# Optimization experiments

Measured on AMD Instinct MI355X. Metric: run time of the kernel, lower is better.

The kernel has to match this reference:

```python
import jax, jax.numpy as jnp
import numpy as np

EPS = 1e-6
L, H, D, DFF = 4, 6, 6, 64  # n_layers, num_heads(=dim, head_dim=1), d_hid, ffn hidden


def layernorm(x, w, b):
    mu = jnp.mean(x, axis=-1, keepdims=True)
    var = jnp.mean((x - mu) ** 2, axis=-1, keepdims=True)
    return (x - mu) / jnp.sqrt(var + EPS) * w + b


def autocorr(x, qw, qb, kw, kb, vw, vb, l1w, l1b):
    # x: [B,S,H]; head_dim==1 so per-head Linear is scalar w*x+b per head.
    k_in = jnp.concatenate([x[:, :1], x[:, :-1]], axis=1)   # roll right, first row kept
    v_in = jnp.concatenate([x[:, 1:], x[:, -1:]], axis=1)   # roll left, last row kept
    q = x * qw + qb
    k = k_in * kw + kb
    v = v_in * vw + vb
    teo = q * q - k * v                                      # [B,S,H]
    # nn.LayerNorm([1]) over size-1 axis: mean==x, var==0 -> output is bias
    normed = (teo - teo) / jnp.sqrt(EPS) * l1w + l1b
    scores = jax.nn.softmax(normed, axis=1)                  # over seq dim
    return scores * teo


def mha(x, p, li, ai):
    out = autocorr(x, p['qw'][li, ai], p['qb'][li, ai], p['kw'][li, ai],
                   p['kb'][li, ai], p['vw'][li, ai], p['vb'][li, ai],
                   p['ln1_w'][li, ai], p['ln1_b'][li, ai])
    return layernorm(out + x, p['mha_ln_w'][li, ai], p['mha_ln_b'][li, ai])


def setup_inputs() -> dict:
    key = jax.random.key(0)
    ks = jax.random.split(key, 24)
    n = jax.random.normal
    inp = {
        'x_batch': n(ks[0], (128, 4096, 6), jnp.float32),
        'enc_output': n(ks[1], (128, 4096, 6), jnp.float32),
        'dec_ln_w': jnp.ones((D,), jnp.float32),
        'dec_ln_b': jnp.zeros((D,), jnp.float32),
        'qw': n(ks[2], (L, 2, H), jnp.float32),
        'qb': n(ks[3], (L, 2, H), jnp.float32) * 0.1,
        'kw': n(ks[4], (L, 2, H), jnp.float32),
        'kb': n(ks[5], (L, 2, H), jnp.float32) * 0.1,
        'vw': n(ks[6], (L, 2, H), jnp.float32),
        'vb': n(ks[7], (L, 2, H), jnp.float32) * 0.1,
        'ln1_w': jnp.ones((L, 2), jnp.float32),
        'ln1_b': jnp.zeros((L, 2), jnp.float32),
        'mha_ln_w': jnp.ones((L, 2, D), jnp.float32),
        'mha_ln_b': jnp.zeros((L, 2, D), jnp.float32),
        'ffn_w1': n(ks[8], (L, DFF, D), jnp.float32) * (1.0 / np.sqrt(D)),
        'ffn_b1': jnp.zeros((L, DFF), jnp.float32),
        'ffn_w2': n(ks[9], (L, D, DFF), jnp.float32) * (1.0 / np.sqrt(DFF)),
        'ffn_b2': jnp.zeros((L, D), jnp.float32),
        'ffn_ln_w': jnp.ones((L, D), jnp.float32),
        'ffn_ln_b': jnp.zeros((L, D), jnp.float32),
    }
    return inp


def reference(x_batch, enc_output, dec_ln_w, dec_ln_b, qw, qb, kw, kb, vw, vb,
              ln1_w, ln1_b, mha_ln_w, mha_ln_b, ffn_w1, ffn_b1, ffn_w2, ffn_b2,
              ffn_ln_w, ffn_ln_b):
    p = dict(qw=qw, qb=qb, kw=kw, kb=kb, vw=vw, vb=vb, ln1_w=ln1_w, ln1_b=ln1_b,
             mha_ln_w=mha_ln_w, mha_ln_b=mha_ln_b)
    x = layernorm(x_batch, dec_ln_w, dec_ln_b)  # dropout p=0 -> identity
    for li in range(L):
        x = mha(x, p, li, 0)   # self-attention block
        x = mha(x, p, li, 1)   # "enc" attention block (also self, per source)
        h = jax.nn.relu(jnp.einsum('bsd,fd->bsf', x, ffn_w1[li]) + ffn_b1[li])
        y = jnp.einsum('bsf,df->bsd', h, ffn_w2[li]) + ffn_b2[li] + x
        x = layernorm(y, ffn_ln_w[li], ffn_ln_b[li])
    return x
```

## Files before the change

### kernel.cpp

```cpp
#include <hip/hip_runtime.h>

#define S_LEN  4096
#define DM     6
#define NLAYER 4
#define NFF    64
#define HALO   8
#define TPB    128
#define OUT_PER_WAVE 112
#define BLK_X 19

typedef float    vf2 __attribute__((ext_vector_type(2)));
typedef float    vf4 __attribute__((ext_vector_type(4)));
typedef _Float16 vh4 __attribute__((ext_vector_type(4)));
typedef _Float16 vh8 __attribute__((ext_vector_type(8)));

#define XSZ (128*16)
#define YSTRIDE 132
#define YSZ (DM*YSTRIDE*4)
#define WAVE_LDS (XSZ + YSZ)

__device__ __forceinline__ vf2 splat2(float s){ vf2 r; r.x = s; r.y = s; return r; }
__device__ __forceinline__ unsigned pkh(float a, float b){
    return __builtin_bit_cast(unsigned, __builtin_amdgcn_cvt_pkrtz(a, b));
}

__device__ __forceinline__ void ln6v(vf2* v, const float* __restrict__ w,
                                     const float* __restrict__ b) {
    vf2 mu = (((v[0]+v[1])+(v[2]+v[3]))+(v[4]+v[5])) * (1.0f/6.0f);
    vf2 var = splat2(0.0f);
#pragma unroll
    for (int d = 0; d < DM; ++d) { vf2 dd = v[d]-mu; var = __builtin_elementwise_fma(dd, dd, var); }
    vf2 a = var * (1.0f/6.0f) + splat2(1e-6f);
    vf2 r; r.x = rsqrtf(a.x); r.y = rsqrtf(a.y);
#pragma unroll
    for (int d = 0; d < DM; ++d)
        v[d] = __builtin_elementwise_fma((v[d]-mu)*r, splat2(w[d]), splat2(b[d]));
}

__global__ __launch_bounds__(TPB, 5)
void decoder_fused(const float* __restrict__ x_batch,
                   const float* __restrict__ dec_ln_w, const float* __restrict__ dec_ln_b,
                   const float* __restrict__ qw, const float* __restrict__ qb,
                   const float* __restrict__ kw, const float* __restrict__ kb,
                   const float* __restrict__ vw, const float* __restrict__ vb,
                   const float* __restrict__ mha_ln_w, const float* __restrict__ mha_ln_b,
                   const float* __restrict__ ffn_w1, const float* __restrict__ ffn_b1,
                   const float* __restrict__ ffn_w2, const float* __restrict__ ffn_b2,
                   const float* __restrict__ ffn_ln_w, const float* __restrict__ ffn_ln_b,
                   float* __restrict__ out) {
    const int lane = threadIdx.x & 63;
    const int wid  = threadIdx.x >> 6;
    const int w    = blockIdx.x * (TPB/64) + wid;
    const int b    = blockIdx.y;
    const int p    = w * OUT_PER_WAVE - HALO + 2*lane;
    const int c    = lane & 15, g = lane >> 4;

    __shared__ __align__(16) char smem[(TPB/64) * WAVE_LDS];
    char* wbase = smem + wid * WAVE_LDS;
    char* Xb = wbase;
    char* Yb = wbase + XSZ;

    vf2 x2[DM];
    if (p >= 0 && p + 1 < S_LEN) {
        const float4* s = reinterpret_cast<const float4*>(x_batch + ((size_t)b*S_LEN + p)*DM);
        float4 a0 = s[0], a1 = s[1], a2 = s[2];
        x2[0].x=a0.x; x2[1].x=a0.y; x2[2].x=a0.z; x2[3].x=a0.w; x2[4].x=a1.x; x2[5].x=a1.y;
        x2[0].y=a1.z; x2[1].y=a1.w; x2[2].y=a2.x; x2[3].y=a2.y; x2[4].y=a2.z; x2[5].y=a2.w;
    } else {
        const int pc = min(max(p, 0), S_LEN-1);
        const float2* s = reinterpret_cast<const float2*>(x_batch + ((size_t)b*S_LEN + pc)*DM);
        float2 a0 = s[0], a1 = s[1], a2 = s[2];
        x2[0] = splat2(a0.x); x2[1] = splat2(a0.y); x2[2] = splat2(a1.x);
        x2[3] = splat2(a1.y); x2[4] = splat2(a2.x); x2[5] = splat2(a2.y);
    }

    ln6v(x2, dec_ln_w, dec_ln_b);

#pragma unroll 1
    for (int li = 0; li < NLAYER; ++li) {
        vh8 w1f[4]; vf4 b1f[4]; vh8 w2f[2];
#pragma unroll
        for (int mt = 0; mt < 4; ++mt) {
            uint4 ua = make_uint4(0u, 0u, 0u, 0u);
            if (g == 0) {
                const float* wr = ffn_w1 + li*NFF*DM + (mt*16 + c)*DM;
                float2 u0 = *reinterpret_cast<const float2*>(wr);
                float2 u1 = *reinterpret_cast<const float2*>(wr + 2);
                float2 u2 = *reinterpret_cast<const float2*>(wr + 4);
                ua = make_uint4(pkh(u0.x,u0.y), pkh(u1.x,u1.y), pkh(u2.x,u2.y), 0u);
            }
            w1f[mt] = __builtin_bit_cast(vh8, ua);

            float4 bb = *reinterpret_cast<const float4*>(ffn_b1 + li*NFF + mt*16 + g*4);
            vf4 bv; bv.x=bb.x; bv.y=bb.y; bv.z=bb.z; bv.w=bb.w;
            b1f[mt] = bv;
        }
#pragma unroll
        for (int ks = 0; ks < 2; ++ks) {
            uint4 uw = make_uint4(0u, 0u, 0u, 0u);
            if (c < DM) {
                const float* wr = ffn_w2 + li*DM*NFF + c*NFF + ks*32 + g*4;
                float4 a0 = *reinterpret_cast<const float4*>(wr);
                float4 a1 = *reinterpret_cast<const float4*>(wr + 16);
                uw = make_uint4(pkh(a0.x,a0.y), pkh(a0.z,a0.w), pkh(a1.x,a1.y), pkh(a1.z,a1.w));
            }
            w2f[ks] = __builtin_bit_cast(vh8, uw);
        }

#pragma unroll 1
        for (int ai = 0; ai < 2; ++ai) {
            const int base = (li*2 + ai) * DM;
            vf2 xm[DM], xp[DM];
#pragma unroll
            for (int d = 0; d < DM; ++d) {
                float up = __shfl_up (x2[d].y, 1);
                float dn = __shfl_down(x2[d].x, 1);
                xm[d].x = (p <= 0) ? x2[d].x : up;
                xm[d].y = x2[d].x;
                xp[d].x = x2[d].y;
                xp[d].y = (p + 1 >= S_LEN - 1) ? x2[d].y : dn;
            }
#pragma unroll
            for (int d = 0; d < DM; ++d) {
                vf2 q = __builtin_elementwise_fma(x2[d], splat2(qw[base+d]), splat2(qb[base+d]));
                vf2 k = __builtin_elementwise_fma(xm[d], splat2(kw[base+d]), splat2(kb[base+d]));
                vf2 v = __builtin_elementwise_fma(xp[d], splat2(vw[base+d]), splat2(vb[base+d]));
                vf2 teo = __builtin_elementwise_fma(q, q, -(k*v));
                x2[d] = __builtin_elementwise_fma(teo, splat2(1.0f/(float)S_LEN), x2[d]);
            }
            ln6v(x2, mha_ln_w + base, mha_ln_b + base);
        }

        {
            {
                char* r0 = Xb + lane*32;
                *(uint4*)r0      = make_uint4(pkh(x2[0].x,x2[1].x), pkh(x2[2].x,x2[3].x),
                                              pkh(x2[4].x,x2[5].x), 0u);
                *(uint4*)(r0+16) = make_uint4(pkh(x2[0].y,x2[1].y), pkh(x2[2].y,x2[3].y),
                                              pkh(x2[4].y,x2[5].y), 0u);
            }
#pragma unroll 2
            for (int t = 0; t < 8; ++t) {
                vh8 bfrag = (vh8)(_Float16)0;
                if (g == 0) bfrag = *(const vh8*)(Xb + (16*t + c)*16);

                vf4 yacc; yacc.x=0.f; yacc.y=0.f; yacc.z=0.f; yacc.w=0.f;
#pragma unroll
                for (int ks = 0; ks < 2; ++ks) {
                    vf4 h0 = __builtin_amdgcn_mfma_f32_16x16x32_f16(w1f[2*ks+0], bfrag, b1f[2*ks+0], 0, 0, 0);
                    vf4 h1 = __builtin_amdgcn_mfma_f32_16x16x32_f16(w1f[2*ks+1], bfrag, b1f[2*ks+1], 0, 0, 0);
                    uint4 hu = make_uint4(pkh(h0.x,h0.y), pkh(h0.z,h0.w),
                                          pkh(h1.x,h1.y), pkh(h1.z,h1.w));
                    vh8 hb = __builtin_bit_cast(vh8, hu);
                    hb = __builtin_elementwise_max(hb, (vh8)(_Float16)0);
                    yacc = __builtin_amdgcn_mfma_f32_16x16x32_f16(hb, w2f[ks], yacc, 0, 0, 0);
                }
                if (c < DM) {
                    float* yp = (float*)Yb + c*YSTRIDE + 16*t + g*4;
                    *reinterpret_cast<vf4*>(yp) = yacc;
                }
            }
            const float* b2 = ffn_b2 + li*DM;
#pragma unroll
            for (int d = 0; d < DM; ++d) {
                float2 yv = *(const float2*)((float*)Yb + d*YSTRIDE + 2*lane);
                vf2 t2; t2.x = yv.x; t2.y = yv.y;
                x2[d] = x2[d] + splat2(b2[d]) + t2;
            }
            ln6v(x2, ffn_ln_w + li*DM, ffn_ln_b + li*DM);
        }
    }

    if (lane >= 4 && lane < 60 && p < S_LEN) {
        float4* dst = reinterpret_cast<float4*>(out + ((size_t)b*S_LEN + p)*DM);
        float4 a0, a1, a2;
        a0.x=x2[0].x; a0.y=x2[1].x; a0.z=x2[2].x; a0.w=x2[3].x;
        a1.x=x2[4].x; a1.y=x2[5].x; a1.z=x2[0].y; a1.w=x2[1].y;
        a2.x=x2[2].y; a2.y=x2[3].y; a2.z=x2[4].y; a2.w=x2[5].y;
        dst[0]=a0; dst[1]=a1; dst[2]=a2;
    }
}

extern "C" void kernel_launch(void* const* d_in, const int* in_sizes, int n_in,
                              void* d_out, int out_size, void* d_ws, size_t ws_size,
                              hipStream_t stream) {
    const float* x_batch  = (const float*)d_in[0];
    const float* dec_ln_w = (const float*)d_in[2];
    const float* dec_ln_b = (const float*)d_in[3];
    const float* qw       = (const float*)d_in[4];
    const float* qb       = (const float*)d_in[5];
    const float* kw       = (const float*)d_in[6];
    const float* kb       = (const float*)d_in[7];
    const float* vw       = (const float*)d_in[8];
    const float* vb       = (const float*)d_in[9];
    const float* mha_ln_w = (const float*)d_in[12];
    const float* mha_ln_b = (const float*)d_in[13];
    const float* ffn_w1   = (const float*)d_in[14];
    const float* ffn_b1   = (const float*)d_in[15];
    const float* ffn_w2   = (const float*)d_in[16];
    const float* ffn_b2   = (const float*)d_in[17];
    const float* ffn_ln_w = (const float*)d_in[18];
    const float* ffn_ln_b = (const float*)d_in[19];
    float* out = (float*)d_out;

    const int B = in_sizes[0] / (S_LEN * DM);
    dim3 grid(BLK_X, B);
    decoder_fused<<<grid, TPB, 0, stream>>>(
        x_batch, dec_ln_w, dec_ln_b, qw, qb, kw, kb, vw, vb,
        mha_ln_w, mha_ln_b, ffn_w1, ffn_b1, ffn_w2, ffn_b2,
        ffn_ln_w, ffn_ln_b, out);
}
```

Baseline: 139.9 us.

## Switch to one token per lane and fold FFN bias into MFMA operand

Each lane now handles one sequence position instead of two, so a wave produces 48 outputs with an 8-token halo on each side instead of 112, and the grid grows to 43 blocks per row. The scalar path drops the packed float2 code, halves per-wave LDS and registers, and the launch bounds target 8 waves per SIMD instead of 5 to raise occupancy. The first FFN bias is folded into the MFMA by adding a constant-1 input column and a bias weight column, which removes the bias accumulator registers. In exchange, halo recomputation overhead rises from 16/128 to 16/64 of the work, and the bias is now rounded to fp16.

```diff
diff --git a/kernel.cpp b/kernel.cpp
--- a/kernel.cpp
+++ b/kernel.cpp
@@ -6,38 +6,35 @@
 #define NFF    64
 #define HALO   8
 #define TPB    128
-#define OUT_PER_WAVE 112
-#define BLK_X 19
+#define OUT_PER_WAVE 48
+#define WAVES_PER_ROW 86
+#define BLK_X 43
 
-typedef float    vf2 __attribute__((ext_vector_type(2)));
 typedef float    vf4 __attribute__((ext_vector_type(4)));
-typedef _Float16 vh4 __attribute__((ext_vector_type(4)));
 typedef _Float16 vh8 __attribute__((ext_vector_type(8)));
 
-#define XSZ (128*16)
-#define YSTRIDE 132
+#define XSZ (64*16)
+#define YSTRIDE 68
 #define YSZ (DM*YSTRIDE*4)
 #define WAVE_LDS (XSZ + YSZ)
 
-__device__ __forceinline__ vf2 splat2(float s){ vf2 r; r.x = s; r.y = s; return r; }
 __device__ __forceinline__ unsigned pkh(float a, float b){
     return __builtin_bit_cast(unsigned, __builtin_amdgcn_cvt_pkrtz(a, b));
 }
 
-__device__ __forceinline__ void ln6v(vf2* v, const float* __restrict__ w,
+__device__ __forceinline__ void ln6s(float* v, const float* __restrict__ w,
                                      const float* __restrict__ b) {
-    vf2 mu = (((v[0]+v[1])+(v[2]+v[3]))+(v[4]+v[5])) * (1.0f/6.0f);
-    vf2 var = splat2(0.0f);
+    float mu = (((v[0]+v[1])+(v[2]+v[3]))+(v[4]+v[5])) * (1.0f/6.0f);
+    float var = 0.0f;
 #pragma unroll
-    for (int d = 0; d < DM; ++d) { vf2 dd = v[d]-mu; var = __builtin_elementwise_fma(dd, dd, var); }
-    vf2 a = var * (1.0f/6.0f) + splat2(1e-6f);
-    vf2 r; r.x = rsqrtf(a.x); r.y = rsqrtf(a.y);
+    for (int d = 0; d < DM; ++d) { float dd = v[d]-mu; var = fmaf(dd, dd, var); }
+    float r = rsqrtf(var * (1.0f/6.0f) + 1e-6f);
 #pragma unroll
     for (int d = 0; d < DM; ++d)
-        v[d] = __builtin_elementwise_fma((v[d]-mu)*r, splat2(w[d]), splat2(b[d]));
+        v[d] = fmaf((v[d]-mu)*r, w[d], b[d]);
 }
 
-__global__ __launch_bounds__(TPB, 5)
+__global__ __launch_bounds__(TPB, 8)
 void decoder_fused(const float* __restrict__ x_batch,
                    const float* __restrict__ dec_ln_w, const float* __restrict__ dec_ln_b,
                    const float* __restrict__ qw, const float* __restrict__ qb,
@@ -52,7 +49,7 @@
     const int wid  = threadIdx.x >> 6;
     const int w    = blockIdx.x * (TPB/64) + wid;
     const int b    = blockIdx.y;
-    const int p    = w * OUT_PER_WAVE - HALO + 2*lane;
+    const int p    = w * OUT_PER_WAVE - HALO + lane;
     const int c    = lane & 15, g = lane >> 4;
 
     __shared__ __align__(16) char smem[(TPB/64) * WAVE_LDS];
@@ -60,25 +57,19 @@
     char* Xb = wbase;
     char* Yb = wbase + XSZ;
 
-    vf2 x2[DM];
-    if (p >= 0 && p + 1 < S_LEN) {
-        const float4* s = reinterpret_cast<const float4*>(x_batch + ((size_t)b*S_LEN + p)*DM);
-        float4 a0 = s[0], a1 = s[1], a2 = s[2];
-        x2[0].x=a0.x; x2[1].x=a0.y; x2[2].x=a0.z; x2[3].x=a0.w; x2[4].x=a1.x; x2[5].x=a1.y;
-        x2[0].y=a1.z; x2[1].y=a1.w; x2[2].y=a2.x; x2[3].y=a2.y; x2[4].y=a2.z; x2[5].y=a2.w;
-    } else {
+    float x[DM];
+    {
         const int pc = min(max(p, 0), S_LEN-1);
         const float2* s = reinterpret_cast<const float2*>(x_batch + ((size_t)b*S_LEN + pc)*DM);
         float2 a0 = s[0], a1 = s[1], a2 = s[2];
-        x2[0] = splat2(a0.x); x2[1] = splat2(a0.y); x2[2] = splat2(a1.x);
-        x2[3] = splat2(a1.y); x2[4] = splat2(a2.x); x2[5] = splat2(a2.y);
+        x[0]=a0.x; x[1]=a0.y; x[2]=a1.x; x[3]=a1.y; x[4]=a2.x; x[5]=a2.y;
     }
 
-    ln6v(x2, dec_ln_w, dec_ln_b);
+    ln6s(x, dec_ln_w, dec_ln_b);
 
 #pragma unroll 1
     for (int li = 0; li < NLAYER; ++li) {
-        vh8 w1f[4]; vf4 b1f[4]; vh8 w2f[2];
+        vh8 w1f[4]; vh8 w2f[2];
 #pragma unroll
         for (int mt = 0; mt < 4; ++mt) {
             uint4 ua = make_uint4(0u, 0u, 0u, 0u);
@@ -87,13 +78,10 @@
                 float2 u0 = *reinterpret_cast<const float2*>(wr);
                 float2 u1 = *reinterpret_cast<const float2*>(wr + 2);
                 float2 u2 = *reinterpret_cast<const float2*>(wr + 4);
-                ua = make_uint4(pkh(u0.x,u0.y), pkh(u1.x,u1.y), pkh(u2.x,u2.y), 0u);
+                float bias = ffn_b1[li*NFF + mt*16 + c];
+                ua = make_uint4(pkh(u0.x,u0.y), pkh(u1.x,u1.y), pkh(u2.x,u2.y), pkh(bias, 0.f));
             }
             w1f[mt] = __builtin_bit_cast(vh8, ua);
-
-            float4 bb = *reinterpret_cast<const float4*>(ffn_b1 + li*NFF + mt*16 + g*4);
-            vf4 bv; bv.x=bb.x; bv.y=bb.y; bv.z=bb.z; bv.w=bb.w;
-            b1f[mt] = bv;
         }
 #pragma unroll
         for (int ks = 0; ks < 2; ++ks) {
@@ -110,45 +98,35 @@
 #pragma unroll 1
         for (int ai = 0; ai < 2; ++ai) {
             const int base = (li*2 + ai) * DM;
-            vf2 xm[DM], xp[DM];
 #pragma unroll
             for (int d = 0; d < DM; ++d) {
-                float up = __shfl_up (x2[d].y, 1);
-                float dn = __shfl_down(x2[d].x, 1);
-                xm[d].x = (p <= 0) ? x2[d].x : up;
-                xm[d].y = x2[d].x;
-                xp[d].x = x2[d].y;
-                xp[d].y = (p + 1 >= S_LEN - 1) ? x2[d].y : dn;
+                float up = __shfl_up (x[d], 1);
+                float dn = __shfl_down(x[d], 1);
+                float xm = (p <= 0)         ? x[d] : up;
+                float xp = (p >= S_LEN - 1) ? x[d] : dn;
+                float q = fmaf(x[d], qw[base+d], qb[base+d]);
+                float k = fmaf(xm,   kw[base+d], kb[base+d]);
+                float v = fmaf(xp,   vw[base+d], vb[base+d]);
+                float teo = fmaf(q, q, -(k*v));
+                x[d] = fmaf(teo, 1.0f/(float)S_LEN, x[d]);
             }
-#pragma unroll
-            for (int d = 0; d < DM; ++d) {
-                vf2 q = __builtin_elementwise_fma(x2[d], splat2(qw[base+d]), splat2(qb[base+d]));
-                vf2 k = __builtin_elementwise_fma(xm[d], splat2(kw[base+d]), splat2(kb[base+d]));
-                vf2 v = __builtin_elementwise_fma(xp[d], splat2(vw[base+d]), splat2(vb[base+d]));
-                vf2 teo = __builtin_elementwise_fma(q, q, -(k*v));
-                x2[d] = __builtin_elementwise_fma(teo, splat2(1.0f/(float)S_LEN), x2[d]);
-            }
-            ln6v(x2, mha_ln_w + base, mha_ln_b + base);
+            ln6s(x, mha_ln_w + base, mha_ln_b + base);
         }
 
         {
-            {
-                char* r0 = Xb + lane*32;
-                *(uint4*)r0      = make_uint4(pkh(x2[0].x,x2[1].x), pkh(x2[2].x,x2[3].x),
-                                              pkh(x2[4].x,x2[5].x), 0u);
-                *(uint4*)(r0+16) = make_uint4(pkh(x2[0].y,x2[1].y), pkh(x2[2].y,x2[3].y),
-                                              pkh(x2[4].y,x2[5].y), 0u);
-            }
-#pragma unroll 2
-            for (int t = 0; t < 8; ++t) {
+            *(uint4*)(Xb + lane*16) = make_uint4(pkh(x[0],x[1]), pkh(x[2],x[3]),
+                                                 pkh(x[4],x[5]), 0x00003C00u);
+#pragma unroll 1
+            for (int t = 0; t < 4; ++t) {
                 vh8 bfrag = (vh8)(_Float16)0;
                 if (g == 0) bfrag = *(const vh8*)(Xb + (16*t + c)*16);
 
                 vf4 yacc; yacc.x=0.f; yacc.y=0.f; yacc.z=0.f; yacc.w=0.f;
 #pragma unroll
                 for (int ks = 0; ks < 2; ++ks) {
-                    vf4 h0 = __builtin_amdgcn_mfma_f32_16x16x32_f16(w1f[2*ks+0], bfrag, b1f[2*ks+0], 0, 0, 0);
-                    vf4 h1 = __builtin_amdgcn_mfma_f32_16x16x32_f16(w1f[2*ks+1], bfrag, b1f[2*ks+1], 0, 0, 0);
+                    vf4 z4; z4.x=0.f; z4.y=0.f; z4.z=0.f; z4.w=0.f;
+                    vf4 h0 = __builtin_amdgcn_mfma_f32_16x16x32_f16(w1f[2*ks+0], bfrag, z4, 0, 0, 0);
+                    vf4 h1 = __builtin_amdgcn_mfma_f32_16x16x32_f16(w1f[2*ks+1], bfrag, z4, 0, 0, 0);
                     uint4 hu = make_uint4(pkh(h0.x,h0.y), pkh(h0.z,h0.w),
                                           pkh(h1.x,h1.y), pkh(h1.z,h1.w));
                     vh8 hb = __builtin_bit_cast(vh8, hu);
@@ -162,22 +140,17 @@
             }
             const float* b2 = ffn_b2 + li*DM;
 #pragma unroll
-            for (int d = 0; d < DM; ++d) {
-                float2 yv = *(const float2*)((float*)Yb + d*YSTRIDE + 2*lane);
-                vf2 t2; t2.x = yv.x; t2.y = yv.y;
-                x2[d] = x2[d] + splat2(b2[d]) + t2;
-            }
-            ln6v(x2, ffn_ln_w + li*DM, ffn_ln_b + li*DM);
+            for (int d = 0; d < DM; ++d)
+                x[d] = x[d] + b2[d] + ((const float*)Yb)[d*YSTRIDE + lane];
+            ln6s(x, ffn_ln_w + li*DM, ffn_ln_b + li*DM);
         }
     }
 
-    if (lane >= 4 && lane < 60 && p < S_LEN) {
-        float4* dst = reinterpret_cast<float4*>(out + ((size_t)b*S_LEN + p)*DM);
-        float4 a0, a1, a2;
-        a0.x=x2[0].x; a0.y=x2[1].x; a0.z=x2[2].x; a0.w=x2[3].x;
-        a1.x=x2[4].x; a1.y=x2[5].x; a1.z=x2[0].y; a1.w=x2[1].y;
-        a2.x=x2[2].y; a2.y=x2[3].y; a2.z=x2[4].y; a2.w=x2[5].y;
-        dst[0]=a0; dst[1]=a1; dst[2]=a2;
+    if (lane >= HALO && lane < HALO + OUT_PER_WAVE && p < S_LEN) {
+        float2* dst = reinterpret_cast<float2*>(out + ((size_t)b*S_LEN + p)*DM);
+        float2 o0, o1, o2;
+        o0.x=x[0]; o0.y=x[1]; o1.x=x[2]; o1.y=x[3]; o2.x=x[4]; o2.y=x[5];
+        dst[0]=o0; dst[1]=o1; dst[2]=o2;
     }
 }
 
```

New measurement: 147.3 us. +5.3%, slower.
